# Kernel tuning notes

Hardware: AMD Instinct MI355X
Metric: run time of the kernel (lower is better)

## Reference

```python
import jax, jax.numpy as jnp
import numpy as np

ROPE_BASE = 10000.0
NEG_INF = -1e30

def _apply_rope(x):
    # x: [B, H, T, D]; interleaved-pair RoPE (torchtune style), positions along axis -2.
    B, H, T, D = x.shape
    inv_freq = 1.0 / (ROPE_BASE ** (jnp.arange(0, D, 2, dtype=jnp.float32) / D))  # [D/2]
    ang = jnp.arange(T, dtype=jnp.float32)[:, None] * inv_freq[None, :]           # [T, D/2]
    cos, sin = jnp.cos(ang), jnp.sin(ang)
    x1, x2 = x[..., 0::2], x[..., 1::2]                                           # [B,H,T,D/2]
    rot = jnp.stack([x1 * cos - x2 * sin, x1 * sin + x2 * cos], axis=-1)          # [B,H,T,D/2,2]
    return rot.reshape(B, H, T, D).astype(x.dtype)

def setup_inputs() -> dict:
    key = jax.random.key(0)
    ks = jax.random.split(key, 5)
    B, T, C = 2, 2048, 1024
    s = 1.0 / np.sqrt(C)
    return {
        "x":  jax.random.normal(ks[0], (B, T, C), jnp.float32),
        "Wq": jax.random.normal(ks[1], (C, C), jnp.float32) * s,
        "bq": jnp.zeros((C,), jnp.float32),
        "Wk": jax.random.normal(ks[2], (C, C), jnp.float32) * s,
        "bk": jnp.zeros((C,), jnp.float32),
        "Wv": jax.random.normal(ks[3], (C, C), jnp.float32) * s,
        "bv": jnp.zeros((C,), jnp.float32),
        "Wo": jax.random.normal(ks[4], (C, C), jnp.float32) * s,
        "bo": jnp.zeros((C,), jnp.float32),
    }

def reference(x, Wq, bq, Wk, bk, Wv, bv, Wo, bo):
    B, T, C = x.shape
    H = 16
    D = C // H
    # QKV projections (torch Linear: x @ W.T + b), split heads -> [B, H, T, D]
    def proj(W, b):
        return (jnp.einsum('btc,oc->bto', x, W) + b).reshape(B, T, H, D).transpose(0, 2, 1, 3)
    q = _apply_rope(proj(Wq, bq))
    k = _apply_rope(proj(Wk, bk))
    v = proj(Wv, bv)
    # Causal scaled dot-product attention
    scale = 1.0 / jnp.sqrt(jnp.asarray(D, x.dtype))
    scores = jnp.einsum('bhqd,bhkd->bhqk', q, k) * scale                          # [B,H,T,T]
    causal = jnp.tril(jnp.ones((T, T), dtype=bool))
    scores = jnp.where(causal, scores, NEG_INF)
    probs = jax.nn.softmax(scores, axis=-1)
    y = jnp.einsum('bhqk,bhkd->bhqd', probs, v)                                   # [B,H,T,D]
    y = y.transpose(0, 2, 1, 3).reshape(B, T, C)
    # Output projection (dropout is identity in eval mode)
    return jnp.einsum('btc,oc->bto', y, Wo) + bo
```

## Files before the change

kernel.cpp:

```cpp
#include <hip/hip_runtime.h>

#define BB 2
#define TT 2048
#define CC 1024
#define HH 16
#define DD 64
#define KDIM 1024
#define MROWS (BB*TT)

typedef __attribute__((ext_vector_type(8))) short  frag_b16;
typedef __attribute__((ext_vector_type(4))) float  f32x4;
typedef __attribute__((ext_vector_type(4))) unsigned short us4;
typedef __attribute__((ext_vector_type(8))) unsigned short us8;
typedef __attribute__((ext_vector_type(4))) _Float16 f16x4;
typedef __attribute__((ext_vector_type(8))) _Float16 f16x8;

#define EXP2F(x) __builtin_amdgcn_exp2f(x)

__device__ __forceinline__ unsigned short f2bf(float f) {
    unsigned int u = __builtin_bit_cast(unsigned int, f);
    u += 0x7FFFu + ((u >> 16) & 1u);
    return (unsigned short)(u >> 16);
}

__device__ __forceinline__ void gl_lds16(const void* g, void* l) {
    __builtin_amdgcn_global_load_lds(
        (const __attribute__((address_space(1))) unsigned int*)g,
        (__attribute__((address_space(3))) unsigned int*)l, 16, 0, 0);
}

__global__ __launch_bounds__(256) void cvt_all(
        const float* __restrict__ x,  const float* __restrict__ w0,
        const float* __restrict__ w1, const float* __restrict__ w2,
        const float* __restrict__ w3, unsigned short* __restrict__ dst) {
    const size_t NX = (size_t)MROWS * CC;
    const size_t NW = (size_t)CC * CC;
    size_t i = ((size_t)blockIdx.x * 256 + threadIdx.x) * 4;
    const float* src; size_t off;
    if (i < NX) { src = x; off = i; }
    else {
        size_t j = i - NX;
        int t = (int)(j >> 20);
        src = (t == 0) ? w0 : (t == 1) ? w1 : (t == 2) ? w2 : w3;
        off = j & (NW - 1);
    }
    float4 f = *reinterpret_cast<const float4*>(src + off);
    us4 o;
    o.x = f2bf(f.x); o.y = f2bf(f.y); o.z = f2bf(f.z); o.w = f2bf(f.w);
    *reinterpret_cast<us4*>(dst + i) = o;
}

__global__ __launch_bounds__(512, 1) void qkv_gemm_rope(
        const unsigned short* __restrict__ X,
        const unsigned short* __restrict__ Wq,
        const unsigned short* __restrict__ Wk,
        const unsigned short* __restrict__ Wv,
        const float* __restrict__ bq, const float* __restrict__ bk,
        const float* __restrict__ bv,
        unsigned short* __restrict__ Qo,
        unsigned short* __restrict__ Ko,
        _Float16* __restrict__ VTo)
{
    const int z = blockIdx.z;
    const unsigned short* W = (z == 0) ? Wq : (z == 1) ? Wk : Wv;
    const float* bias = (z == 0) ? bq : (z == 1) ? bk : bv;

    const int tid = threadIdx.x;
    const int w = tid >> 6;
    const int lane = tid & 63;
    const int l16 = lane & 15;
    const int quad = lane >> 4;
    const int wm = w >> 2;
    const int wn = w & 3;

    const int bx = blockIdx.x * 256;
    const int by = blockIdx.y * 256;
    const int rowbase = bx + wm * 128;
    const int colbase = by + wn * 64;

    __shared__ __align__(16) char smem[131072];
    unsigned short* Ab = (unsigned short*)smem;
    unsigned short* Bb = (unsigned short*)(smem + 65536);
    _Float16 (*Vl)[64][72] = (_Float16(*)[64][72])smem;

    f32x4 acc[8][4] = {};

    const int nB0 = (tid & 255) + ((tid >> 8) << 9);

    {
        const int an[4] = { tid, tid + 512, tid + 1024, tid + 1536 };
        const int bn[4] = { nB0, nB0 + 256, nB0 + 1024, nB0 + 1280 };
#pragma unroll
        for (int i = 0; i < 4; ++i) {
            int r = an[i] >> 3, cc_ = ((an[i] & 7) ^ (r & 7)) * 8;
            gl_lds16(X + (size_t)(bx + r) * KDIM + cc_, Ab + an[i] * 8);
            r = bn[i] >> 3; cc_ = ((bn[i] & 7) ^ (r & 7)) * 8;
            gl_lds16(W + (size_t)(by + r) * KDIM + cc_, Bb + bn[i] * 8);
        }
    }
    asm volatile("s_waitcnt vmcnt(0)" ::: "memory");
    __builtin_amdgcn_s_barrier();

    frag_b16 bC[4][2], bN[4][2];
#pragma unroll
    for (int c = 0; c < 4; ++c) {
        const int row = wn * 64 + c * 16 + l16;
        const unsigned short* Br = Bb + row * 64;
#pragma unroll
        for (int kh = 0; kh < 2; ++kh) {
            const int sl = (kh * 4 + quad) ^ (row & 7);
            bC[c][kh] = *reinterpret_cast<const frag_b16*>(Br + sl * 8);
        }
    }

    auto ktile = [&](int t, int bsel, frag_b16 (&bA)[4][2], frag_b16 (&bNx)[4][2]) {
        const bool pre = (t + 1 < 16);
        const int kk = (t + 1) * 64;
        const unsigned short* Ac = Ab + bsel * 16384;
        unsigned short* An = Ab + (bsel ^ 1) * 16384;
        unsigned short* Bn = Bb + (bsel ^ 1) * 16384;
#pragma unroll
        for (int q = 0; q < 4; ++q) {
            frag_b16 a[2][2];
#pragma unroll
            for (int m = 0; m < 2; ++m) {
                const int row = wm * 128 + q * 32 + m * 16 + l16;
                const unsigned short* Ar = Ac + row * 64;
#pragma unroll
                for (int kh = 0; kh < 2; ++kh) {
                    const int sl = (kh * 4 + quad) ^ (row & 7);
                    a[m][kh] = *reinterpret_cast<const frag_b16*>(Ar + sl * 8);
                }
            }
            if (q >= 2 && pre) {
#pragma unroll
                for (int hh = 0; hh < 2; ++hh) {
                    const int c = (q - 2) * 2 + hh;
                    const int row = wn * 64 + c * 16 + l16;
                    const unsigned short* Br = Bn + row * 64;
#pragma unroll
                    for (int kh = 0; kh < 2; ++kh) {
                        const int sl = (kh * 4 + quad) ^ (row & 7);
                        bNx[c][kh] = *reinterpret_cast<const frag_b16*>(Br + sl * 8);
                    }
                }
            }
            if (pre) {
                int n0, n1; const unsigned short* G; unsigned short* L; int g0;
                if (q == 0)      { n0 = nB0;        n1 = nB0 + 1024; G = W; L = Bn; g0 = by; }
                else if (q == 1) { n0 = nB0 + 256;  n1 = nB0 + 1280; G = W; L = Bn; g0 = by; }
                else if (q == 2) { n0 = tid;        n1 = tid + 1024; G = X; L = An; g0 = bx; }
                else             { n0 = tid + 512;  n1 = tid + 1536; G = X; L = An; g0 = bx; }
                {   int r = n0 >> 3, cc_ = ((n0 & 7) ^ (r & 7)) * 8;
                    gl_lds16(G + (size_t)(g0 + r) * KDIM + kk + cc_, L + n0 * 8); }
                {   int r = n1 >> 3, cc_ = ((n1 & 7) ^ (r & 7)) * 8;
                    gl_lds16(G + (size_t)(g0 + r) * KDIM + kk + cc_, L + n1 * 8); }
            }
            __builtin_amdgcn_s_barrier();
            __builtin_amdgcn_s_setprio(1);
#pragma unroll
            for (int m = 0; m < 2; ++m)
#pragma unroll
                for (int c = 0; c < 4; ++c) {
                    acc[q * 2 + m][c] = __builtin_amdgcn_mfma_f32_16x16x32_bf16(
                        a[m][0], bA[c][0], acc[q * 2 + m][c], 0, 0, 0);
                    acc[q * 2 + m][c] = __builtin_amdgcn_mfma_f32_16x16x32_bf16(
                        a[m][1], bA[c][1], acc[q * 2 + m][c], 0, 0, 0);
                }
            __builtin_amdgcn_s_setprio(0);
            asm volatile("s_waitcnt vmcnt(2)" ::: "memory");
            __builtin_amdgcn_s_barrier();
        }
    };

#pragma unroll 1
    for (int tt = 0; tt < 8; ++tt) {
        ktile(2 * tt,     0, bC, bN);
        ktile(2 * tt + 1, 1, bN, bC);
    }

    if (z == 2) {
        const int b_ = rowbase >> 11;
        const int h  = colbase >> 6;
        const int dl = lane >> 3;
        const int t8 = (lane & 7) * 8;
#pragma unroll
        for (int hp = 0; hp < 2; ++hp) {
#pragma unroll
            for (int r4 = 0; r4 < 4; ++r4) {
                const int r = hp * 4 + r4;
#pragma unroll
                for (int c = 0; c < 4; ++c) {
                    f16x4 pk;
#pragma unroll
                    for (int g = 0; g < 4; ++g)
                        pk[g] = (_Float16)(acc[r][c][g] + bias[colbase + c * 16 + l16]);
                    *reinterpret_cast<f16x4*>(
                        &Vl[w][c * 16 + l16][r4 * 16 + quad * 4]) = pk;
                }
            }
            __builtin_amdgcn_s_waitcnt(0);
#pragma unroll
            for (int i = 0; i < 8; ++i) {
                const int d = i * 8 + dl;
                f16x8 v = *reinterpret_cast<const f16x8*>(&Vl[w][d][t8]);
                *reinterpret_cast<f16x8*>(
                    &VTo[((size_t)(b_ * HH + h) * DD + d) * TT
                         + (rowbase & (TT - 1)) + hp * 64 + t8]) = v;
            }
            __builtin_amdgcn_s_waitcnt(0);
        }
    } else {
        const float qsc = (z == 0) ? 0.180336888f : 1.0f;
        unsigned short* dst = (z == 0) ? Qo : Ko;
        const int b_ = rowbase >> 11;
        const int tq0 = (rowbase & (TT - 1)) + quad * 4;
#pragma unroll
        for (int c = 0; c < 4; ++c) {
            const int o = colbase + c * 16 + l16;
            const int h = o >> 6, d = o & (DD - 1);
            const float inv = __expf(-(float)(d & ~1) * (9.210340371976184f / (float)DD));
            float cs0, sn0, cs1, sn1, cs16, sn16;
            __sincosf((float)tq0 * inv, &sn0, &cs0);
            __sincosf(inv, &sn1, &cs1);
            __sincosf(16.f * inv, &sn16, &cs16);
            float cr = cs0, sr = sn0;
#pragma unroll
            for (int r = 0; r < 8; ++r) {
                float cg = cr, sg = sr;
#pragma unroll
                for (int g = 0; g < 4; ++g) {
                    int n = rowbase + r * 16 + quad * 4 + g;
                    int t = n & (TT - 1);
                    float v = acc[r][c][g] + bias[o];
                    float pv = __shfl_xor(v, 1);
                    float outv = (d & 1) ? (pv * sg + v * cg) : (v * cg - pv * sg);
                    dst[((size_t)(b_ * HH + h) * TT + t) * DD + d] = f2bf(outv * qsc);
                    float cn = cg * cs1 - sg * sn1;
                    sg = sg * cs1 + cg * sn1;
                    cg = cn;
                }
                float crn = cr * cs16 - sr * sn16;
                sr = sr * cs16 + cr * sn16;
                cr = crn;
            }
        }
    }
}

__global__ __launch_bounds__(256, 2) void attn(
        const unsigned short* __restrict__ Q,
        const unsigned short* __restrict__ K,
        const _Float16* __restrict__ VT,
        unsigned short* __restrict__ Y)
{
    const int b1d = blockIdx.x;
    const int bh = (b1d & 7) * 4 + ((b1d >> 3) & 3);
    const int pair = b1d >> 5;
    const int tid = threadIdx.x;
    const int w = tid >> 6;
    const int lane = tid & 63;
    const int l16 = lane & 15;
    const int quad = lane >> 4;

    const unsigned short* Qp = Q + (size_t)bh * TT * DD;
    const unsigned short* Kp = K + (size_t)bh * TT * DD;
    const _Float16* Vp = VT + (size_t)bh * DD * TT;

    __shared__ unsigned short Kl[2][128][64];
    __shared__ _Float16 Vl[2][64][128];
    __shared__ unsigned short Ylds[4][16][72];

    const int sw = (l16 & 7);
    const int b_ = bh >> 4, h = bh & (HH - 1);

    f16x4 ones;
    ones[0] = ones[1] = ones[2] = ones[3] = (_Float16)1.0f;

#pragma unroll 1
    for (int seg = 0; seg < 2; ++seg) {
        const int qblk = seg ? (31 - pair) : pair;
        const int q0 = qblk * 64;
        const int q = q0 + w * 16 + l16;

        frag_b16 bq[2];
#pragma unroll
        for (int dk = 0; dk < 2; ++dk)
            bq[dk] = *reinterpret_cast<const frag_b16*>(
                Qp + (size_t)q * DD + dk * 32 + quad * 8);

        f32x4 yacc[4] = {};
        f32x4 lsum = {};

        const int ntiles = (qblk >> 1) + 1;

#pragma unroll
        for (int i = 0; i < 4; ++i) {
            int n = tid + 256 * i;
            int kr = n >> 3,  kc = ((n & 7)  ^ (kr & 7)) * 8;
            int vr = n >> 4,  vc = ((n & 15) ^ (vr & 7)) * 8;
            gl_lds16(Kp + (size_t)kr * DD + kc, (unsigned short*)&Kl[0][0][0] + n * 8);
            gl_lds16(Vp + (size_t)vr * TT + vc, (_Float16*)&Vl[0][0][0] + n * 8);
        }

#pragma unroll 1
        for (int it = 0; it < ntiles; ++it) {
            __syncthreads();
            const int bsel = it & 1;
            if (it + 1 < ntiles) {
                const int jn = (it + 1) * 128;
                const int bn = bsel ^ 1;
#pragma unroll
                for (int i = 0; i < 4; ++i) {
                    int n = tid + 256 * i;
                    int kr = n >> 3,  kc = ((n & 7)  ^ (kr & 7)) * 8;
                    int vr = n >> 4,  vc = ((n & 15) ^ (vr & 7)) * 8;
                    gl_lds16(Kp + (size_t)(jn + kr) * DD + kc,
                             (unsigned short*)&Kl[bn][0][0] + n * 8);
                    gl_lds16(Vp + (size_t)vr * TT + jn + vc,
                             (_Float16*)&Vl[bn][0][0] + n * 8);
                }
            }
            const int j0 = it * 128;

            f32x4 s[8];
#pragma unroll
            for (int mt = 0; mt < 8; ++mt) {
                frag_b16 ak0 = *reinterpret_cast<const frag_b16*>(
                    &Kl[bsel][mt * 16 + l16][(quad ^ sw) * 8]);
                frag_b16 ak1 = *reinterpret_cast<const frag_b16*>(
                    &Kl[bsel][mt * 16 + l16][((4 + quad) ^ sw) * 8]);
                f32x4 t = {};
                t = __builtin_amdgcn_mfma_f32_16x16x32_bf16(ak0, bq[0], t, 0, 0, 0);
                t = __builtin_amdgcn_mfma_f32_16x16x32_bf16(ak1, bq[1], t, 0, 0, 0);
                s[mt] = t;
            }

            if (it == ntiles - 1) {
#pragma unroll
                for (int mt = 0; mt < 8; ++mt)
#pragma unroll
                    for (int g = 0; g < 4; ++g) {
                        int key = j0 + mt * 16 + quad * 4 + g;
                        if (key > q) s[mt][g] = -1e30f;
                    }
            }

            f16x4 pb[8];
#pragma unroll
            for (int mt = 0; mt < 8; ++mt)
#pragma unroll
                for (int g = 0; g < 4; ++g)
                    pb[mt][g] = (_Float16)EXP2F(s[mt][g] - 11.0f);

#pragma unroll
            for (int kt = 0; kt < 8; ++kt)
                lsum = __builtin_amdgcn_mfma_f32_16x16x16f16(ones, pb[kt], lsum, 0, 0, 0);

#pragma unroll
            for (int dt = 0; dt < 4; ++dt) {
                f32x4 ya = yacc[dt];
#pragma unroll
                for (int kt = 0; kt < 8; ++kt) {
                    int colp = (kt * 2 + (quad >> 1)) ^ sw;
                    f16x4 av = *reinterpret_cast<const f16x4*>(
                        &Vl[bsel][dt * 16 + l16][colp * 8 + (quad & 1) * 4]);
                    ya = __builtin_amdgcn_mfma_f32_16x16x16f16(av, pb[kt], ya, 0, 0, 0);
                }
                yacc[dt] = ya;
            }
        }

        __syncthreads();

        float rl = 1.f / lsum[0];
#pragma unroll
        for (int dt = 0; dt < 4; ++dt)
#pragma unroll
            for (int g = 0; g < 4; ++g)
                Ylds[w][l16][dt * 16 + quad * 4 + g] = f2bf(yacc[dt][g] * rl);

#pragma unroll
        for (int i = 0; i < 2; ++i) {
            int idx = i * 64 + lane;
            int r = idx >> 3, c8 = (idx & 7) * 8;
            us8 v = *reinterpret_cast<const us8*>(&Ylds[w][r][c8]);
            *reinterpret_cast<us8*>(
                &Y[(size_t)(b_ * TT + q0 + w * 16 + r) * CC + h * DD + c8]) = v;
        }
    }
}

__global__ __launch_bounds__(256, 2) void out_gemm(
        const unsigned short* __restrict__ Y,
        const unsigned short* __restrict__ Wo,
        const float* __restrict__ bo,
        float* __restrict__ out)
{
    const int tid = threadIdx.x;
    const int wave = tid >> 6;
    const int lane = tid & 63;
    const int l16 = lane & 15;
    const int quad = lane >> 4;

    const int bx = blockIdx.x * 128;
    const int by = blockIdx.y * 128;
    const int row0 = bx + (wave >> 1) * 64;
    const int col0 = by + (wave & 1) * 64;

    __shared__ __align__(16) char smem[65536];
    unsigned short* Xa0 = (unsigned short*)smem;
    unsigned short* Wb0 = (unsigned short*)(smem + 32768);

    f32x4 acc[4][4] = {};

    int srow[4]; int scol[4];
#pragma unroll
    for (int i = 0; i < 4; ++i) {
        int n = tid + 256 * i;
        srow[i] = n >> 3;
        scol[i] = ((n & 7) ^ (srow[i] & 7)) * 8;
    }

#pragma unroll
    for (int i = 0; i < 4; ++i) {
        int n = tid + 256 * i;
        gl_lds16(Y  + (size_t)(bx + srow[i]) * KDIM + scol[i], Xa0 + n * 8);
        gl_lds16(Wo + (size_t)(by + srow[i]) * KDIM + scol[i], Wb0 + n * 8);
    }

    const int ar = (wave >> 1) * 64;
    const int bc = (wave & 1) * 64;

#pragma unroll 1
    for (int step = 0; step < 16; ++step) {
        __syncthreads();
        const int bsel = step & 1;
        if (step + 1 < 16) {
            const int kk = (step + 1) * 64;
            const int bo_ = (bsel ^ 1) * 8192;
#pragma unroll
            for (int i = 0; i < 4; ++i) {
                int n = tid + 256 * i;
                gl_lds16(Y  + (size_t)(bx + srow[i]) * KDIM + kk + scol[i],
                         Xa0 + bo_ + n * 8);
                gl_lds16(Wo + (size_t)(by + srow[i]) * KDIM + kk + scol[i],
                         Wb0 + bo_ + n * 8);
            }
        }

        frag_b16 a[4][2], b[4][2];
#pragma unroll
        for (int r = 0; r < 4; ++r) {
            int row = ar + r * 16 + l16;
#pragma unroll
            for (int kh = 0; kh < 2; ++kh) {
                int c = (kh * 4 + quad) ^ (row & 7);
                a[r][kh] = *reinterpret_cast<const frag_b16*>(
                    Xa0 + bsel * 8192 + row * 64 + c * 8);
            }
        }
#pragma unroll
        for (int cc = 0; cc < 4; ++cc) {
            int row = bc + cc * 16 + l16;
#pragma unroll
            for (int kh = 0; kh < 2; ++kh) {
                int c = (kh * 4 + quad) ^ (row & 7);
                b[cc][kh] = *reinterpret_cast<const frag_b16*>(
                    Wb0 + bsel * 8192 + row * 64 + c * 8);
            }
        }
#pragma unroll
        for (int r = 0; r < 4; ++r)
#pragma unroll
            for (int c = 0; c < 4; ++c) {
                acc[r][c] = __builtin_amdgcn_mfma_f32_16x16x32_bf16(a[r][0], b[c][0], acc[r][c], 0, 0, 0);
                acc[r][c] = __builtin_amdgcn_mfma_f32_16x16x32_bf16(a[r][1], b[c][1], acc[r][c], 0, 0, 0);
            }
    }

#pragma unroll
    for (int r = 0; r < 4; ++r)
#pragma unroll
        for (int c = 0; c < 4; ++c)
#pragma unroll
            for (int g = 0; g < 4; ++g) {
                int n = row0 + r * 16 + quad * 4 + g;
                int o = col0 + c * 16 + l16;
                out[(size_t)n * CC + o] = acc[r][c][g] + bo[o];
            }
}

extern "C" void kernel_launch(void* const* d_in, const int* in_sizes, int n_in,
                              void* d_out, int out_size, void* d_ws, size_t ws_size,
                              hipStream_t stream) {
    const float* x  = (const float*)d_in[0];
    const float* Wq = (const float*)d_in[1];
    const float* bq = (const float*)d_in[2];
    const float* Wk = (const float*)d_in[3];
    const float* bk = (const float*)d_in[4];
    const float* Wv = (const float*)d_in[5];
    const float* bv = (const float*)d_in[6];
    const float* Wo = (const float*)d_in[7];
    const float* bo = (const float*)d_in[8];
    float* out = (float*)d_out;

    unsigned short* ws = (unsigned short*)d_ws;
    const size_t NX = (size_t)MROWS * CC;
    const size_t NW = (size_t)CC * CC;
    unsigned short* xb  = ws;
    unsigned short* wqb = xb  + NX;
    unsigned short* wkb = wqb + NW;
    unsigned short* wvb = wkb + NW;
    unsigned short* wob = wvb + NW;
    unsigned short* Qr  = wob + NW;
    unsigned short* Kr  = Qr  + NX;
    _Float16*       VTb = (_Float16*)(Kr + NX);
    unsigned short* Yb  = (unsigned short*)(VTb + NX);

    const size_t NALL = NX + 4 * NW;
    cvt_all<<<dim3((unsigned)(NALL / 1024)), 256, 0, stream>>>(x, Wq, Wk, Wv, Wo, xb);

    qkv_gemm_rope<<<dim3(MROWS / 256, CC / 256, 3), 512, 0, stream>>>(
        xb, wqb, wkb, wvb, bq, bk, bv, Qr, Kr, VTb);

    attn<<<dim3(512), 256, 0, stream>>>(Qr, Kr, VTb, Yb);

    out_gemm<<<dim3(MROWS / 128, CC / 128), 256, 0, stream>>>(Yb, wob, bo, out);
}
```

Measured before the change: 176.6 us.

## Reorder projection GEMM k-tile into 4x2 quadrants with current-buffer B fragments

Restructures the projection GEMM inner k-tile loop. Each wave now works on 4 M-fragments × 2 N-fragments per phase and loads its B fragments from the current LDS buffer, rather than carrying B fragments prefetched from the next buffer across tiles. The global-to-LDS prefetch issues are regrouped unevenly across phases, with per-phase vmcnt waits tuned to match. This is meant to cut register pressure and better overlap LDS reads with MFMA work. In exchange, the hand-counted waitcnt values are fragile and could introduce races or extra stalls.

```diff
diff --git a/kernel.cpp b/kernel.cpp
--- a/kernel.cpp
+++ b/kernel.cpp
@@ -101,82 +101,137 @@
     asm volatile("s_waitcnt vmcnt(0)" ::: "memory");
     __builtin_amdgcn_s_barrier();
 
-    frag_b16 bC[4][2], bN[4][2];
-#pragma unroll
-    for (int c = 0; c < 4; ++c) {
-        const int row = wn * 64 + c * 16 + l16;
-        const unsigned short* Br = Bb + row * 64;
-#pragma unroll
-        for (int kh = 0; kh < 2; ++kh) {
-            const int sl = (kh * 4 + quad) ^ (row & 7);
-            bC[c][kh] = *reinterpret_cast<const frag_b16*>(Br + sl * 8);
-        }
-    }
-
-    auto ktile = [&](int t, int bsel, frag_b16 (&bA)[4][2], frag_b16 (&bNx)[4][2]) {
+    auto ktile = [&](int t, int bsel) {
         const bool pre = (t + 1 < 16);
         const int kk = (t + 1) * 64;
         const unsigned short* Ac = Ab + bsel * 16384;
+        const unsigned short* Bc = Bb + bsel * 16384;
         unsigned short* An = Ab + (bsel ^ 1) * 16384;
         unsigned short* Bn = Bb + (bsel ^ 1) * 16384;
+
+        frag_b16 a[4][2], b01[2][2], b23[2][2];
+
 #pragma unroll
         for (int q = 0; q < 4; ++q) {
-            frag_b16 a[2][2];
-#pragma unroll
-            for (int m = 0; m < 2; ++m) {
-                const int row = wm * 128 + q * 32 + m * 16 + l16;
-                const unsigned short* Ar = Ac + row * 64;
-#pragma unroll
-                for (int kh = 0; kh < 2; ++kh) {
-                    const int sl = (kh * 4 + quad) ^ (row & 7);
-                    a[m][kh] = *reinterpret_cast<const frag_b16*>(Ar + sl * 8);
-                }
-            }
-            if (q >= 2 && pre) {
-#pragma unroll
-                for (int hh = 0; hh < 2; ++hh) {
-                    const int c = (q - 2) * 2 + hh;
-                    const int row = wn * 64 + c * 16 + l16;
-                    const unsigned short* Br = Bn + row * 64;
+            if (q == 0) {
+#pragma unroll
+                for (int m = 0; m < 4; ++m) {
+                    const int row = wm * 128 + m * 16 + l16;
+                    const unsigned short* Ar = Ac + row * 64;
 #pragma unroll
                     for (int kh = 0; kh < 2; ++kh) {
                         const int sl = (kh * 4 + quad) ^ (row & 7);
-                        bNx[c][kh] = *reinterpret_cast<const frag_b16*>(Br + sl * 8);
+                        a[m][kh] = *reinterpret_cast<const frag_b16*>(Ar + sl * 8);
+                    }
+                }
+#pragma unroll
+                for (int c = 0; c < 2; ++c) {
+                    const int row = wn * 64 + c * 16 + l16;
+                    const unsigned short* Br = Bc + row * 64;
+#pragma unroll
+                    for (int kh = 0; kh < 2; ++kh) {
+                        const int sl = (kh * 4 + quad) ^ (row & 7);
+                        b01[c][kh] = *reinterpret_cast<const frag_b16*>(Br + sl * 8);
+                    }
+                }
+            } else if (q == 1) {
+#pragma unroll
+                for (int c = 0; c < 2; ++c) {
+                    const int row = wn * 64 + (c + 2) * 16 + l16;
+                    const unsigned short* Br = Bc + row * 64;
+#pragma unroll
+                    for (int kh = 0; kh < 2; ++kh) {
+                        const int sl = (kh * 4 + quad) ^ (row & 7);
+                        b23[c][kh] = *reinterpret_cast<const frag_b16*>(Br + sl * 8);
+                    }
+                }
+            } else if (q == 2) {
+#pragma unroll
+                for (int m = 0; m < 4; ++m) {
+                    const int row = wm * 128 + 64 + m * 16 + l16;
+                    const unsigned short* Ar = Ac + row * 64;
+#pragma unroll
+                    for (int kh = 0; kh < 2; ++kh) {
+                        const int sl = (kh * 4 + quad) ^ (row & 7);
+                        a[m][kh] = *reinterpret_cast<const frag_b16*>(Ar + sl * 8);
                     }
                 }
             }
             if (pre) {
-                int n0, n1; const unsigned short* G; unsigned short* L; int g0;
-                if (q == 0)      { n0 = nB0;        n1 = nB0 + 1024; G = W; L = Bn; g0 = by; }
-                else if (q == 1) { n0 = nB0 + 256;  n1 = nB0 + 1280; G = W; L = Bn; g0 = by; }
-                else if (q == 2) { n0 = tid;        n1 = tid + 1024; G = X; L = An; g0 = bx; }
-                else             { n0 = tid + 512;  n1 = tid + 1536; G = X; L = An; g0 = bx; }
-                {   int r = n0 >> 3, cc_ = ((n0 & 7) ^ (r & 7)) * 8;
-                    gl_lds16(G + (size_t)(g0 + r) * KDIM + kk + cc_, L + n0 * 8); }
-                {   int r = n1 >> 3, cc_ = ((n1 & 7) ^ (r & 7)) * 8;
-                    gl_lds16(G + (size_t)(g0 + r) * KDIM + kk + cc_, L + n1 * 8); }
+                if (q == 0) {
+                    {   int n = tid;          int r = n >> 3, cc_ = ((n & 7) ^ (r & 7)) * 8;
+                        gl_lds16(X + (size_t)(bx + r) * KDIM + kk + cc_, An + n * 8); }
+                    {   int n = tid + 1024;   int r = n >> 3, cc_ = ((n & 7) ^ (r & 7)) * 8;
+                        gl_lds16(X + (size_t)(bx + r) * KDIM + kk + cc_, An + n * 8); }
+                    {   int n = nB0;          int r = n >> 3, cc_ = ((n & 7) ^ (r & 7)) * 8;
+                        gl_lds16(W + (size_t)(by + r) * KDIM + kk + cc_, Bn + n * 8); }
+                    {   int n = nB0 + 1024;   int r = n >> 3, cc_ = ((n & 7) ^ (r & 7)) * 8;
+                        gl_lds16(W + (size_t)(by + r) * KDIM + kk + cc_, Bn + n * 8); }
+                } else if (q == 1) {
+                    {   int n = nB0 + 256;    int r = n >> 3, cc_ = ((n & 7) ^ (r & 7)) * 8;
+                        gl_lds16(W + (size_t)(by + r) * KDIM + kk + cc_, Bn + n * 8); }
+                    {   int n = nB0 + 1280;   int r = n >> 3, cc_ = ((n & 7) ^ (r & 7)) * 8;
+                        gl_lds16(W + (size_t)(by + r) * KDIM + kk + cc_, Bn + n * 8); }
+                } else if (q == 2) {
+                    {   int n = tid + 512;    int r = n >> 3, cc_ = ((n & 7) ^ (r & 7)) * 8;
+                        gl_lds16(X + (size_t)(bx + r) * KDIM + kk + cc_, An + n * 8); }
+                    {   int n = tid + 1536;   int r = n >> 3, cc_ = ((n & 7) ^ (r & 7)) * 8;
+                        gl_lds16(X + (size_t)(bx + r) * KDIM + kk + cc_, An + n * 8); }
+                }
             }
             __builtin_amdgcn_s_barrier();
             __builtin_amdgcn_s_setprio(1);
-#pragma unroll
-            for (int m = 0; m < 2; ++m)
-#pragma unroll
-                for (int c = 0; c < 4; ++c) {
-                    acc[q * 2 + m][c] = __builtin_amdgcn_mfma_f32_16x16x32_bf16(
-                        a[m][0], bA[c][0], acc[q * 2 + m][c], 0, 0, 0);
-                    acc[q * 2 + m][c] = __builtin_amdgcn_mfma_f32_16x16x32_bf16(
-                        a[m][1], bA[c][1], acc[q * 2 + m][c], 0, 0, 0);
-                }
+            if (q == 0) {
+#pragma unroll
+                for (int m = 0; m < 4; ++m)
+#pragma unroll
+                    for (int c = 0; c < 2; ++c) {
+                        acc[m][c] = __builtin_amdgcn_mfma_f32_16x16x32_bf16(a[m][0], b01[c][0], acc[m][c], 0, 0, 0);
+                        acc[m][c] = __builtin_amdgcn_mfma_f32_16x16x32_bf16(a[m][1], b01[c][1], acc[m][c], 0, 0, 0);
+                    }
+            } else if (q == 1) {
+#pragma unroll
+                for (int m = 0; m < 4; ++m)
+#pragma unroll
+                    for (int c = 0; c < 2; ++c) {
+                        acc[m][c + 2] = __builtin_amdgcn_mfma_f32_16x16x32_bf16(a[m][0], b23[c][0], acc[m][c + 2], 0, 0, 0);
+                        acc[m][c + 2] = __builtin_amdgcn_mfma_f32_16x16x32_bf16(a[m][1], b23[c][1], acc[m][c + 2], 0, 0, 0);
+                    }
+            } else if (q == 2) {
+#pragma unroll
+                for (int m = 0; m < 4; ++m)
+#pragma unroll
+                    for (int c = 0; c < 2; ++c) {
+                        acc[m + 4][c] = __builtin_amdgcn_mfma_f32_16x16x32_bf16(a[m][0], b01[c][0], acc[m + 4][c], 0, 0, 0);
+                        acc[m + 4][c] = __builtin_amdgcn_mfma_f32_16x16x32_bf16(a[m][1], b01[c][1], acc[m + 4][c], 0, 0, 0);
+                    }
+            } else {
+#pragma unroll
+                for (int m = 0; m < 4; ++m)
+#pragma unroll
+                    for (int c = 0; c < 2; ++c) {
+                        acc[m + 4][c + 2] = __builtin_amdgcn_mfma_f32_16x16x32_bf16(a[m][0], b23[c][0], acc[m + 4][c + 2], 0, 0, 0);
+                        acc[m + 4][c + 2] = __builtin_amdgcn_mfma_f32_16x16x32_bf16(a[m][1], b23[c][1], acc[m + 4][c + 2], 0, 0, 0);
+                    }
+            }
             __builtin_amdgcn_s_setprio(0);
-            asm volatile("s_waitcnt vmcnt(2)" ::: "memory");
+            if (pre) {
+                if (q == 0)      asm volatile("s_waitcnt vmcnt(6)" ::: "memory");
+                else if (q == 1) asm volatile("s_waitcnt vmcnt(6)" ::: "memory");
+                else if (q == 2) asm volatile("s_waitcnt vmcnt(8)" ::: "memory");
+                else             asm volatile("s_waitcnt vmcnt(4)" ::: "memory");
+            } else {
+                if (q == 0)      asm volatile("s_waitcnt vmcnt(2)" ::: "memory");
+                else if (q == 1) asm volatile("s_waitcnt vmcnt(0)" ::: "memory");
+            }
             __builtin_amdgcn_s_barrier();
         }
     };
 
 #pragma unroll 1
     for (int tt = 0; tt < 8; ++tt) {
-        ktile(2 * tt,     0, bC, bN);
-        ktile(2 * tt + 1, 1, bN, bC);
+        ktile(2 * tt,     0);
+        ktile(2 * tt + 1, 1);
     }
 
     if (z == 2) {
```

Result: no change. 177.1 us (+0.3%).
